# Optimization experiments

Measured on AMD Instinct MI355X. Metric: run time of the kernel, lower is better.

Reference implementation:

```python
import jax, jax.numpy as jnp
import numpy as np

B = 16
D = 512
LENGTHS = [2048 + 256 * i for i in range(B)]  # sum = 63488 tokens (incl. cls per bag)


def _index_maps(lengths):
    # Static (numpy) index maps for ragged <-> padded layout. Each bag's row 0 is a
    # cls token (left untouched); rows 1..L-1 are the conv body.
    lengths = [int(l) for l in np.asarray(lengths).tolist()]
    offs = np.cumsum([0] + lengths)
    lens_b = [l - 1 for l in lengths]            # body lengths after removing cls
    Lmax = max(lens_b)
    Bn = len(lengths)
    pad_src = np.zeros((Bn, Lmax), dtype=np.int32)   # flat x row gathered into [b,t]
    pad_mask = np.zeros((Bn, Lmax), dtype=np.float32)
    body_pos_list, body_b_list, body_t_list = [], [], []
    for i, L in enumerate(lens_b):
        rows = np.arange(offs[i] + 1, offs[i] + 1 + L)
        pad_src[i, :L] = rows
        pad_mask[i, :L] = 1.0
        body_pos_list.append(rows)
        body_b_list.append(np.full(L, i, dtype=np.int32))
        body_t_list.append(np.arange(L, dtype=np.int32))
    body_pos = np.concatenate(body_pos_list)   # flat positions of body tokens
    body_b = np.concatenate(body_b_list)
    body_t = np.concatenate(body_t_list)
    return pad_src, pad_mask, body_pos, body_b, body_t


def _dwconv(xp, w, b):
    # Depthwise 'same' conv1d. xp: [B, D, Lmax], w: [D, 1, k] (torch layout), b: [D].
    y = jax.lax.conv_general_dilated(
        xp, w, window_strides=(1,), padding='SAME',
        feature_group_count=xp.shape[1],
        dimension_numbers=('NCH', 'OIH', 'NCH'))
    return y + b[None, :, None]


def setup_inputs():
    key = jax.random.key(0)
    ks = jax.random.split(key, 7)
    total = sum(LENGTHS)
    x = jax.random.normal(ks[0], (total, D), jnp.float32)
    def u(k, shape, fan):  # torch Conv1d default init: U(-1/sqrt(fan_in*k), ...)
        bound = 1.0 / np.sqrt(fan)
        return jax.random.uniform(k, shape, jnp.float32, -bound, bound)
    w3, b3 = u(ks[1], (D, 1, 3), 3), u(ks[2], (D,), 3)
    w5, b5 = u(ks[3], (D, 1, 5), 5), u(ks[4], (D,), 5)
    w7, b7 = u(ks[5], (D, 1, 7), 7), u(ks[6], (D,), 7)
    lengths = np.array(LENGTHS, dtype=np.int64)
    return {'x': x, 'w3': w3, 'b3': b3, 'w5': w5, 'b5': b5,
            'w7': w7, 'b7': b7, 'lengths': lengths}


def reference(x, w3, b3, w5, b5, w7, b7, lengths):
    pad_src, pad_mask, body_pos, body_b, body_t = _index_maps(lengths)
    # Gather ragged bodies into zero-padded [B, Lmax, D]; zero padding reproduces
    # the per-segment 'same' conv boundary behavior exactly.
    xb = x[pad_src] * pad_mask[:, :, None]
    xp = jnp.transpose(xb, (0, 2, 1))  # [B, D, Lmax]
    y = xp + _dwconv(xp, w3, b3) + _dwconv(xp, w5, b5) + _dwconv(xp, w7, b7)
    body = jnp.transpose(y, (0, 2, 1))[body_b, body_t]  # flat [sum(len-1), D]
    # cls rows keep original x values; body rows replaced by residual conv sum.
    return x.at[body_pos].set(body)
```

## Files before the change

### kernel.cpp

```cpp
#include <hip/hip_runtime.h>

#define DCH 512
#define RPB 16
#define NW  (RPB + 6)

typedef float f32x4 __attribute__((ext_vector_type(4)));

__global__ __launch_bounds__(128) void ppeg_dwconv_kernel(
    const float* __restrict__ x,
    const float* __restrict__ w3, const float* __restrict__ b3,
    const float* __restrict__ w5, const float* __restrict__ b5,
    const float* __restrict__ w7, const float* __restrict__ b7,
    const int* __restrict__ lengths,
    float* __restrict__ out, int n_rows, int n_bags, int nblocks)
{
    __shared__ int soff[40];

    const int tid = threadIdx.x;
    const int c0  = tid * 4;

    int bid = blockIdx.x;
    {
        const int nx = 8;
        const int q  = nblocks / nx, rm = nblocks % nx;
        const int xcd = bid % nx, idx = bid / nx;
        bid = (xcd < rm ? xcd * (q + 1) : rm * (q + 1) + (xcd - rm) * q) + idx;
    }
    const int r0 = bid * RPB;
    if (r0 >= n_rows) return;

    float4 win[NW];
    if (r0 >= 3 && r0 + RPB + 2 < n_rows) {
        const float* xp = x + (size_t)(r0 - 3) * DCH + c0;
        #pragma unroll
        for (int j = 0; j < NW; ++j)
            win[j] = *(const float4*)(xp + (size_t)j * DCH);
    } else {
        #pragma unroll
        for (int j = 0; j < NW; ++j) {
            const int rr = r0 - 3 + j;
            win[j] = (rr >= 0 && rr < n_rows)
                       ? *(const float4*)(x + (size_t)rr * DCH + c0)
                       : make_float4(0.f, 0.f, 0.f, 0.f);
        }
    }

    if (tid == 0) {
        int acc = 0;
        for (int i = 0; i < n_bags; ++i) { soff[i] = acc; acc += lengths[i]; }
        soff[n_bags] = acc;
    }

    float W[7][4], bias[4];
    #pragma unroll
    for (int q2 = 0; q2 < 4; ++q2) {
        const int d = c0 + q2;
        const float a0 = w7[d*7+0], a1 = w7[d*7+1], a2 = w7[d*7+2], a3 = w7[d*7+3],
                    a4 = w7[d*7+4], a5 = w7[d*7+5], a6 = w7[d*7+6];
        const float f0 = w5[d*5+0], f1 = w5[d*5+1], f2 = w5[d*5+2], f3 = w5[d*5+3], f4 = w5[d*5+4];
        const float e0 = w3[d*3+0], e1 = w3[d*3+1], e2 = w3[d*3+2];
        W[0][q2] = a0;
        W[1][q2] = a1 + f0;
        W[2][q2] = a2 + f1 + e0;
        W[3][q2] = a3 + f2 + e1 + 1.0f;
        W[4][q2] = a4 + f3 + e2;
        W[5][q2] = a5 + f4;
        W[6][q2] = a6;
        bias[q2] = b3[d] + b5[d] + b7[d];
    }

    __syncthreads();

    int b = 0;
    #pragma unroll
    for (int s = 16; s >= 1; s >>= 1)
        if (b + s < n_bags && soff[b + s] <= r0) b += s;

    const int e0b = soff[b];
    const int e1b = soff[b + 1];
    const int e2b = (b + 2 <= n_bags) ? soff[b + 2] : e1b;

    #pragma unroll
    for (int i = 0; i < RPB; ++i) {
        const int r = r0 + i;
        if (r < n_rows) {
            const bool nb   = (r >= e1b);
            const int  offb = nb ? e1b : e0b;
            const int  endb = nb ? e2b : e1b;
            const int  t    = r - offb - 1;
            const int  Lb1  = endb - offb - 1;

            float4 o;
            if (t < 0) {
                o = win[i + 3];
            } else if (t >= 3 && t + 3 < Lb1) {
                float a0 = bias[0], a1 = bias[1], a2 = bias[2], a3 = bias[3];
                #pragma unroll
                for (int dt = 0; dt < 7; ++dt) {
                    const float4 v = win[i + dt];
                    a0 = fmaf(W[dt][0], v.x, a0);
                    a1 = fmaf(W[dt][1], v.y, a1);
                    a2 = fmaf(W[dt][2], v.z, a2);
                    a3 = fmaf(W[dt][3], v.w, a3);
                }
                o = make_float4(a0, a1, a2, a3);
            } else {
                float a0 = bias[0], a1 = bias[1], a2 = bias[2], a3 = bias[3];
                #pragma unroll
                for (int dt = 0; dt < 7; ++dt) {
                    const int  tp    = t + dt - 3;
                    const bool valid = (tp >= 0) && (tp < Lb1);
                    const float mm   = valid ? 1.0f : 0.0f;
                    const float4 v = win[i + dt];
                    a0 = fmaf(mm * W[dt][0], v.x, a0);
                    a1 = fmaf(mm * W[dt][1], v.y, a1);
                    a2 = fmaf(mm * W[dt][2], v.z, a2);
                    a3 = fmaf(mm * W[dt][3], v.w, a3);
                }
                o = make_float4(a0, a1, a2, a3);
            }

            f32x4 ov = {o.x, o.y, o.z, o.w};
            __builtin_nontemporal_store(ov, (f32x4*)(out + (size_t)r * DCH + c0));
        }
    }
}

extern "C" void kernel_launch(void* const* d_in, const int* in_sizes, int n_in,
                              void* d_out, int out_size, void* d_ws, size_t ws_size,
                              hipStream_t stream) {
    const float* x       = (const float*)d_in[0];
    const float* w3      = (const float*)d_in[1];
    const float* b3      = (const float*)d_in[2];
    const float* w5      = (const float*)d_in[3];
    const float* b5      = (const float*)d_in[4];
    const float* w7      = (const float*)d_in[5];
    const float* b7      = (const float*)d_in[6];
    const int*   lengths = (const int*)d_in[7];

    const int n_bags = in_sizes[7];
    const int n_rows = in_sizes[0] / DCH;
    float* out = (float*)d_out;

    const int nblocks = (n_rows + RPB - 1) / RPB;
    ppeg_dwconv_kernel<<<nblocks, 128, 0, stream>>>(
        x, w3, b3, w5, b5, w7, b7, lengths, out, n_rows, n_bags, nblocks);
}
```

Before: 245.8 us.

## Persistent blocks with triple-buffered async global-to-LDS tile pipeline

```diff
diff --git a/kernel.cpp b/kernel.cpp
--- a/kernel.cpp
+++ b/kernel.cpp
@@ -1,49 +1,58 @@
 #include <hip/hip_runtime.h>
 
-#define DCH 512
-#define RPB 16
-#define NW  (RPB + 6)
+#define DCH    512
+#define RPB    16
+#define WROWS  (RPB + 6)
+#define BUFF   (WROWS * DCH)
+#define CHUNKS (WROWS * 2)
+#define NWAVE  4
+#define TPW    (CHUNKS / NWAVE)
+#define NBLK   256
 
-typedef float f32x4 __attribute__((ext_vector_type(4)));
+typedef float f32x2 __attribute__((ext_vector_type(2)));
 
-__global__ __launch_bounds__(128) void ppeg_dwconv_kernel(
+__device__ __forceinline__ void vmwait(int n) {
+    switch (n) {
+        case 0:  asm volatile("s_waitcnt vmcnt(0)"  ::: "memory"); break;
+        case 22: asm volatile("s_waitcnt vmcnt(22)" ::: "memory"); break;
+        case 38: asm volatile("s_waitcnt vmcnt(38)" ::: "memory"); break;
+        default: asm volatile("s_waitcnt vmcnt(54)" ::: "memory"); break;
+    }
+    __builtin_amdgcn_sched_barrier(0);
+}
+
+__device__ __forceinline__ void stage_tile(const float* __restrict__ x,
+                                           float* lbase, int r0, int n_rows,
+                                           int wid, int lane)
+{
+    #pragma unroll
+    for (int s = 0; s < TPW; ++s) {
+        const int c = wid + NWAVE * s;
+        int row = r0 - 3 + (c >> 1);
+        row = row < 0 ? 0 : (row >= n_rows ? n_rows - 1 : row);
+        const float* g = x + (size_t)row * DCH + (c & 1) * 256 + lane * 4;
+        float* l = lbase + c * 256;
+        __builtin_amdgcn_global_load_lds(
+            (const __attribute__((address_space(1))) void*)g,
+            (__attribute__((address_space(3))) void*)l, 16, 0, 0);
+    }
+}
+
+__global__ __launch_bounds__(256) void ppeg_dwconv_kernel(
     const float* __restrict__ x,
     const float* __restrict__ w3, const float* __restrict__ b3,
     const float* __restrict__ w5, const float* __restrict__ b5,
     const float* __restrict__ w7, const float* __restrict__ b7,
     const int* __restrict__ lengths,
-    float* __restrict__ out, int n_rows, int n_bags, int nblocks)
+    float* __restrict__ out, int n_rows, int n_bags)
 {
+    __shared__ float lbuf[3][BUFF];
     __shared__ int soff[40];
 
-    const int tid = threadIdx.x;
-    const int c0  = tid * 4;
-
-    int bid = blockIdx.x;
-    {
-        const int nx = 8;
-        const int q  = nblocks / nx, rm = nblocks % nx;
-        const int xcd = bid % nx, idx = bid / nx;
-        bid = (xcd < rm ? xcd * (q + 1) : rm * (q + 1) + (xcd - rm) * q) + idx;
-    }
-    const int r0 = bid * RPB;
-    if (r0 >= n_rows) return;
-
-    float4 win[NW];
-    if (r0 >= 3 && r0 + RPB + 2 < n_rows) {
-        const float* xp = x + (size_t)(r0 - 3) * DCH + c0;
-        #pragma unroll
-        for (int j = 0; j < NW; ++j)
-            win[j] = *(const float4*)(xp + (size_t)j * DCH);
-    } else {
-        #pragma unroll
-        for (int j = 0; j < NW; ++j) {
-            const int rr = r0 - 3 + j;
-            win[j] = (rr >= 0 && rr < n_rows)
-                       ? *(const float4*)(x + (size_t)rr * DCH + c0)
-                       : make_float4(0.f, 0.f, 0.f, 0.f);
-        }
-    }
+    const int tid  = threadIdx.x;
+    const int wid  = tid >> 6;
+    const int lane = tid & 63;
+    const int c0   = tid * 2;
 
     if (tid == 0) {
         int acc = 0;
@@ -51,9 +60,9 @@
         soff[n_bags] = acc;
     }
 
-    float W[7][4], bias[4];
+    float W[7][2], bias[2];
     #pragma unroll
-    for (int q2 = 0; q2 < 4; ++q2) {
+    for (int q2 = 0; q2 < 2; ++q2) {
         const int d = c0 + q2;
         const float a0 = w7[d*7+0], a1 = w7[d*7+1], a2 = w7[d*7+2], a3 = w7[d*7+3],
                     a4 = w7[d*7+4], a5 = w7[d*7+5], a6 = w7[d*7+6];
@@ -71,58 +80,84 @@
 
     __syncthreads();
 
-    int b = 0;
-    #pragma unroll
-    for (int s = 16; s >= 1; s >>= 1)
-        if (b + s < n_bags && soff[b + s] <= r0) b += s;
+    const int ntiles = (n_rows + RPB - 1) / RPB;
+    const int nblk   = gridDim.x;
+    const int q      = ntiles / nblk, rem = ntiles % nblk;
+    const int bidx   = blockIdx.x;
+    const int T      = q + (bidx < rem ? 1 : 0);
+    const int t0     = bidx * q + (bidx < rem ? bidx : rem);
+    if (T <= 0) return;
 
-    const int e0b = soff[b];
-    const int e1b = soff[b + 1];
-    const int e2b = (b + 2 <= n_bags) ? soff[b + 2] : e1b;
+    stage_tile(x, &lbuf[0][0], t0 * RPB, n_rows, wid, lane);
+    if (T > 1) stage_tile(x, &lbuf[1][0], (t0 + 1) * RPB, n_rows, wid, lane);
 
-    #pragma unroll
-    for (int i = 0; i < RPB; ++i) {
-        const int r = r0 + i;
-        if (r < n_rows) {
+    for (int k = 0; k < T; ++k) {
+        const int r0 = (t0 + k) * RPB;
+
+        if (k + 2 < T)
+            stage_tile(x, &lbuf[(k + 2) % 3][0], (t0 + k + 2) * RPB, n_rows, wid, lane);
+
+        int b = 0;
+        #pragma unroll
+        for (int s = 16; s >= 1; s >>= 1)
+            if (b + s < n_bags && soff[b + s] <= r0) b += s;
+        const int e0b = soff[b];
+        const int e1b = soff[b + 1];
+        const int e2b = (b + 2 <= n_bags) ? soff[b + 2] : e1b;
+
+        const int w = (k + 2 < T) ? (k == 0 ? 22 : (k == 1 ? 38 : 54)) : 0;
+        vmwait(w);
+        __builtin_amdgcn_s_barrier();
+        __builtin_amdgcn_sched_barrier(0);
+
+        const float* lb = &lbuf[k % 3][0];
+        float*       ob = out + (size_t)r0 * DCH + c0;
+
+        #pragma unroll
+        for (int i = 0; i < RPB; ++i) {
+            const int r = r0 + i;
+
             const bool nb   = (r >= e1b);
             const int  offb = nb ? e1b : e0b;
             const int  endb = nb ? e2b : e1b;
             const int  t    = r - offb - 1;
             const int  Lb1  = endb - offb - 1;
 
-            float4 o;
+            f32x2 v[7];
+            #pragma unroll
+            for (int dt = 0; dt < 7; ++dt)
+                v[dt] = *(const f32x2*)(lb + (i + dt) * DCH + c0);
+
+            f32x2 o;
             if (t < 0) {
-                o = win[i + 3];
+                o = v[3];
             } else if (t >= 3 && t + 3 < Lb1) {
-                float a0 = bias[0], a1 = bias[1], a2 = bias[2], a3 = bias[3];
+                float a0 = bias[0], a1 = bias[1];
                 #pragma unroll
                 for (int dt = 0; dt < 7; ++dt) {
-                    const float4 v = win[i + dt];
-                    a0 = fmaf(W[dt][0], v.x, a0);
-                    a1 = fmaf(W[dt][1], v.y, a1);
-                    a2 = fmaf(W[dt][2], v.z, a2);
-                    a3 = fmaf(W[dt][3], v.w, a3);
+                    a0 = fmaf(W[dt][0], v[dt].x, a0);
+                    a1 = fmaf(W[dt][1], v[dt].y, a1);
                 }
-                o = make_float4(a0, a1, a2, a3);
+                o = (f32x2){a0, a1};
             } else {
-                float a0 = bias[0], a1 = bias[1], a2 = bias[2], a3 = bias[3];
+                float a0 = bias[0], a1 = bias[1];
                 #pragma unroll
                 for (int dt = 0; dt < 7; ++dt) {
                     const int  tp    = t + dt - 3;
-                    const bool valid = (tp >= 0) && (tp < Lb1);
-                    const float mm   = valid ? 1.0f : 0.0f;
-                    const float4 v = win[i + dt];
-                    a0 = fmaf(mm * W[dt][0], v.x, a0);
-                    a1 = fmaf(mm * W[dt][1], v.y, a1);
-                    a2 = fmaf(mm * W[dt][2], v.z, a2);
-                    a3 = fmaf(mm * W[dt][3], v.w, a3);
+                    const float mm   = (tp >= 0 && tp < Lb1) ? 1.0f : 0.0f;
+                    a0 = fmaf(mm * W[dt][0], v[dt].x, a0);
+                    a1 = fmaf(mm * W[dt][1], v[dt].y, a1);
                 }
-                o = make_float4(a0, a1, a2, a3);
+                o = (f32x2){a0, a1};
             }
 
-            f32x4 ov = {o.x, o.y, o.z, o.w};
-            __builtin_nontemporal_store(ov, (f32x4*)(out + (size_t)r * DCH + c0));
+            if (r < n_rows)
+                __builtin_nontemporal_store(o, (f32x2*)(ob + (size_t)i * DCH));
         }
+
+        asm volatile("s_waitcnt lgkmcnt(0)" ::: "memory");
+        __builtin_amdgcn_s_barrier();
+        __builtin_amdgcn_sched_barrier(0);
     }
 }
 
@@ -142,7 +177,8 @@
     const int n_rows = in_sizes[0] / DCH;
     float* out = (float*)d_out;
 
-    const int nblocks = (n_rows + RPB - 1) / RPB;
-    ppeg_dwconv_kernel<<<nblocks, 128, 0, stream>>>(
-        x, w3, b3, w5, b5, w7, b7, lengths, out, n_rows, n_bags, nblocks);
+    const int ntiles = (n_rows + RPB - 1) / RPB;
+    const int nblk   = ntiles < NBLK ? ntiles : NBLK;
+    ppeg_dwconv_kernel<<<nblk, 256, 0, stream>>>(
+        x, w3, b3, w5, b5, w7, b7, lengths, out, n_rows, n_bags);
 }
```

After: 251.0 us. +2.1%, slower.
